# Performance work log

Hardware: AMD Instinct MI355X
Metric: run time of the kernel (lower is better)

## Reference

```python
import jax, jax.numpy as jnp
import numpy as np

L, B, D, H, DM = 4, 32768, 64, 256, 32
NS = 8            # fixed RK4 steps standing in for adaptive Dormand-Prince (atol=1e-5)
EPS = 1e-3        # keras BatchNormalization epsilon


def setup_inputs() -> dict:
    key = jax.random.key(0)
    ks = jax.random.split(key, 16)
    g = lambda k, shape, s=0.05: jax.random.normal(k, shape, jnp.float32) * s
    perm = jnp.concatenate([jnp.arange(DM, D), jnp.arange(DM)]).astype(jnp.int32)
    return {
        'x': jax.random.normal(ks[0], (B, D), jnp.float32),
        'perms': jnp.tile(perm[None, :], (L, 1)),
        'nvp_W0': g(ks[1], (L, DM, H)), 'nvp_b0': jnp.zeros((L, H), jnp.float32),
        'nvp_W1': g(ks[2], (L, H, H)), 'nvp_b1': jnp.zeros((L, H), jnp.float32),
        'nvp_W2': g(ks[3], (L, H, 2 * (D - DM))), 'nvp_b2': jnp.zeros((L, 2 * (D - DM)), jnp.float32),
        'ode_W0': g(ks[4], (L, D + 1, H)), 'ode_b0': jnp.zeros((L, H), jnp.float32),
        'ode_W1': g(ks[5], (L, H, H)), 'ode_b1': jnp.zeros((L, H), jnp.float32),
        'ode_W2': g(ks[6], (L, H, D)), 'ode_b2': jnp.zeros((L, D), jnp.float32),
        'bn1_mean': g(ks[7], (L, D), 0.1), 'bn1_var': jax.random.uniform(ks[8], (L, D), jnp.float32, 0.5, 1.5),
        'bn1_gamma': jax.random.uniform(ks[9], (L, D), jnp.float32, 0.8, 1.2), 'bn1_beta': g(ks[10], (L, D), 0.1),
        'bn2_mean': g(ks[11], (L, D), 0.1), 'bn2_var': jax.random.uniform(ks[12], (L, D), jnp.float32, 0.5, 1.5),
        'bn2_gamma': jax.random.uniform(ks[13], (L, D), jnp.float32, 0.8, 1.2), 'bn2_beta': g(ks[14], (L, D), 0.1),
    }


def _nvp(x, W0, b0, W1, b1, W2, b2):
    # RealNVP coupling: pass-through masked half, affine-transform the rest
    x0, x1 = x[:, :DM], x[:, DM:]
    h = jax.nn.relu(x0 @ W0 + b0)
    h = jax.nn.relu(h @ W1 + b1)
    shift, log_scale = jnp.split(h @ W2 + b2, 2, axis=-1)
    return jnp.concatenate([x0, x1 * jnp.exp(log_scale) + shift], axis=-1)


def _bn_fwd(x, mean, var, gamma, beta):
    # TFP BatchNormalization bijector forward == de-normalization
    return (x - beta) * jnp.sqrt(var + EPS) / gamma + mean


def _ffjord(x, W0, b0, W1, b1, W2, b2):
    # integrate dx/dt = MLP([t, x]) from t=0 to t=1 (fixed-step RK4)
    def f(t, y):
        ty = jnp.concatenate([jnp.full((y.shape[0], 1), t, y.dtype), y], axis=-1)
        h = jnp.tanh(ty @ W0 + b0)
        h = jnp.tanh(h @ W1 + b1)
        return h @ W2 + b2

    dt = 1.0 / NS

    def step(y, t):
        k1 = f(t, y)
        k2 = f(t + dt / 2, y + (dt / 2) * k1)
        k3 = f(t + dt / 2, y + (dt / 2) * k2)
        k4 = f(t + dt, y + dt * k3)
        return y + (dt / 6) * (k1 + 2 * k2 + 2 * k3 + k4), None

    ts = jnp.arange(NS, dtype=x.dtype) * dt
    y, _ = jax.lax.scan(step, x, ts)
    return y


def reference(x, perms, nvp_W0, nvp_b0, nvp_W1, nvp_b1, nvp_W2, nvp_b2,
              ode_W0, ode_b0, ode_W1, ode_b1, ode_W2, ode_b2,
              bn1_mean, bn1_var, bn1_gamma, bn1_beta,
              bn2_mean, bn2_var, bn2_gamma, bn2_beta):
    for i in range(L):  # per layer: Permute -> RealNVP -> BN -> FFJORD -> BN
        x = x[:, perms[i]]
        x = _nvp(x, nvp_W0[i], nvp_b0[i], nvp_W1[i], nvp_b1[i], nvp_W2[i], nvp_b2[i])
        x = _bn_fwd(x, bn1_mean[i], bn1_var[i], bn1_gamma[i], bn1_beta[i])
        x = _ffjord(x, ode_W0[i], ode_b0[i], ode_W1[i], ode_b1[i], ode_W2[i], ode_b2[i])
        x = _bn_fwd(x, bn2_mean[i], bn2_var[i], bn2_gamma[i], bn2_beta[i])
    return x
```

## Files before the change

### kernel.cpp

```cpp
#include <hip/hip_runtime.h>


#define LNUM   4
#define NSTEP  8
#define EPSV   1e-3f

typedef __attribute__((ext_vector_type(8))) short  short8;
typedef __attribute__((ext_vector_type(4))) float  floatx4;

#define MF(a, b, c) __builtin_amdgcn_mfma_f32_16x16x32_bf16((a), (b), (c), 0, 0, 0)

#define OW0_OFF 0
#define OW1_OFF 65536
#define OW2_OFF 327680
#define NW0_OFF 393216
#define NW1_OFF 425984
#define NW2_OFF 688128
#define WS_ELEMS 753664

#define W1B_OFF  0
#define H1_OFF   81920
#define H2_OFF   98304
#define YIN_OFF  114688
#define X1B_OFF  118784
#define SHF_OFF  120832
#define PARS_OFF 122880
#define LDS_SIZE 126208

__device__ __forceinline__ unsigned short f2bfu(float f) {
  return (unsigned short)((__float_as_uint(f) + 0x8000u) >> 16);
}

__device__ __forceinline__ unsigned short f2bfu_rne(float f) {
  unsigned int u = __float_as_uint(f);
  return (unsigned short)((u + 0x7FFFu + ((u >> 16) & 1u)) >> 16);
}

__device__ __forceinline__ unsigned long long pack4bf(float a, float b, float c, float d) {
  return (unsigned long long)f2bfu(a)
       | ((unsigned long long)f2bfu(b) << 16)
       | ((unsigned long long)f2bfu(c) << 32)
       | ((unsigned long long)f2bfu(d) << 48);
}

__device__ __forceinline__ float bfu2f(unsigned short u) {
  return __uint_as_float((unsigned int)u << 16);
}

__device__ __forceinline__ float tanh_fast(float x) {
  float e = __expf(2.0f * x);
  return 1.0f - 2.0f * __builtin_amdgcn_rcpf(e + 1.0f);
}

__global__ void prep_kernel(const float* __restrict__ odeW0, const float* __restrict__ odeW1,
                            const float* __restrict__ odeW2, const float* __restrict__ nvpW0,
                            const float* __restrict__ nvpW1, const float* __restrict__ nvpW2,
                            unsigned short* __restrict__ ws) {
  int idx = blockIdx.x * blockDim.x + threadIdx.x;
  if (idx >= WS_ELEMS) return;
  const float* W; int base, K, N, lstride, skip;
  int f = idx;
  if (f < OW1_OFF)      { W = odeW0; base = OW0_OFF; K = 64;  N = 256; lstride = 16640; skip = 1; f -= OW0_OFF; }
  else if (f < OW2_OFF) { W = odeW1; base = OW1_OFF; K = 256; N = 256; lstride = 65536; skip = 0; f -= OW1_OFF; }
  else if (f < NW0_OFF) { W = odeW2; base = OW2_OFF; K = 256; N = 64;  lstride = 16384; skip = 0; f -= OW2_OFF; }
  else if (f < NW1_OFF) { W = nvpW0; base = NW0_OFF; K = 32;  N = 256; lstride = 8192;  skip = 0; f -= NW0_OFF; }
  else if (f < NW2_OFF) { W = nvpW1; base = NW1_OFF; K = 256; N = 256; lstride = 65536; skip = 0; f -= NW1_OFF; }
  else                  { W = nvpW2; base = NW2_OFF; K = 256; N = 64;  lstride = 16384; skip = 0; f -= NW2_OFF; }
  int per   = K * N;
  int layer = f / per;
  int e     = f - layer * per;
  int j  = e & 7;
  int l  = (e >> 3) & 63;
  int t  = e >> 9;
  int KS = K >> 5; if (KS < 1) KS = 1;
  int ks = t % KS;
  int nt = t / KS;
  int n = nt * 16 + (l & 15);
  int k = ks * 32 + ((l >> 4) << 3) + j;
  ws[base + layer * per + e] = f2bfu_rne(W[layer * lstride + (k + skip) * N + n]);
}

__device__ __forceinline__ void st_h(char* dst, int m, int n0, float a, float b, float c, float d) {
  int off = (m * 512 + n0 * 2) ^ ((m & 15) << 4);
  *reinterpret_cast<unsigned long long*>(dst + off) = pack4bf(a, b, c, d);
}

__global__ void
__launch_bounds__(512)
flow_kernel(const float* __restrict__ xin,
            const float* __restrict__ nvp_b0, const float* __restrict__ nvp_b1,
            const float* __restrict__ nvp_b2,
            const float* __restrict__ odeW0_full,
            const float* __restrict__ ode_b0, const float* __restrict__ ode_b1,
            const float* __restrict__ ode_b2,
            const float* __restrict__ bn1m, const float* __restrict__ bn1v,
            const float* __restrict__ bn1g, const float* __restrict__ bn1b,
            const float* __restrict__ bn2m, const float* __restrict__ bn2v,
            const float* __restrict__ bn2g, const float* __restrict__ bn2b,
            const unsigned short* __restrict__ ws,
            float* __restrict__ out) {
  __shared__ __align__(16) char smem[LDS_SIZE];
  short8* w1b = reinterpret_cast<short8*>(smem + W1B_OFF);
  char*  h1   = smem + H1_OFF;
  char*  h2   = smem + H2_OFF;
  char*  yinb = smem + YIN_OFF;
  char*  x1b  = smem + X1B_OFF;
  char*  shfb = smem + SHF_OFF;
  float* pars = reinterpret_cast<float*>(smem + PARS_OFF);

  const floatx4 zero4 = {0.f, 0.f, 0.f, 0.f};

  const int tid  = threadIdx.x;
  const int lane = tid & 63;
  const int w    = tid >> 6;
  const int l15  = lane & 15;
  const int g    = lane >> 4;
  const int wn   = w & 3;
  const int wm   = w >> 2;
  const int nb   = w * 32;
  const int mrow = wm * 16 + l15;
  const int row0 = blockIdx.x * 32;
  const int d0   = wn * 16 + g * 4;
  const float dtv = 1.0f / NSTEP;

  float y[4];
  {
    floatx4 v = *reinterpret_cast<const floatx4*>(xin + (row0 + mrow) * 64 + d0);
    y[0] = v[0]; y[1] = v[1]; y[2] = v[2]; y[3] = v[3];
  }

  short8 aw0[2][2];
  short8 aw1h[2][3];
  short8 aw2[8];

  for (int l = 0; l < LNUM; ++l) {
    __syncthreads();
    {
      const short8* src = reinterpret_cast<const short8*>(ws + NW1_OFF + l * 65536);
      #pragma unroll 2
      for (int i = tid; i < 5120; i += 512) {
        int ks3 = i >> 10;
        int rem = i & 1023;
        w1b[i] = src[((rem >> 6) << 9) + ((3 + ks3) << 6) + (rem & 63)];
      }
    }
    if (wn >= 2) {
      int off = (mrow * 128 + (d0 - 32) * 2) ^ ((mrow & 7) << 4);
      *reinterpret_cast<unsigned long long*>(yinb + off) = pack4bf(y[0], y[1], y[2], y[3]);
    } else {
      int off = (mrow * 64 + d0 * 2) ^ ((mrow & 3) << 4);
      *reinterpret_cast<unsigned long long*>(x1b + off) = pack4bf(y[0], y[1], y[2], y[3]);
    }
    for (int i = tid; i < 576; i += 512) {
      float v;
      if (i < 256)      v = nvp_b0[l * 256 + i];
      else if (i < 512) v = nvp_b1[l * 256 + i - 256];
      else              v = nvp_b2[l * 64 + i - 512];
      pars[i] = v;
    }
    {
      const short8* p0 = reinterpret_cast<const short8*>(ws + NW0_OFF + l * 8192);
      const short8* p1 = reinterpret_cast<const short8*>(ws + NW1_OFF + l * 65536);
      const short8* p2 = reinterpret_cast<const short8*>(ws + NW2_OFF + l * 16384);
      aw0[0][0] = p0[(w * 2 + 0) * 64 + lane];
      aw0[1][0] = p0[(w * 2 + 1) * 64 + lane];
      #pragma unroll
      for (int nt = 0; nt < 2; ++nt)
        #pragma unroll
        for (int ks = 0; ks < 3; ++ks) aw1h[nt][ks] = p1[((w * 2 + nt) * 8 + ks) * 64 + lane];
      #pragma unroll
      for (int ks = 0; ks < 8; ++ks) aw2[ks] = p2[(wn * 8 + ks) * 64 + lane];
    }
    __syncthreads();

    {
      floatx4 acc[2][2];
      #pragma unroll
      for (int nt = 0; nt < 2; ++nt)
        #pragma unroll
        for (int mt = 0; mt < 2; ++mt) acc[nt][mt] = zero4;
      short8 B[2];
      #pragma unroll
      for (int mt = 0; mt < 2; ++mt) {
        int m = mt * 16 + l15;
        int off = (m * 128 + g * 16) ^ ((m & 7) << 4);
        B[mt] = *reinterpret_cast<const short8*>(yinb + off);
      }
      #pragma unroll
      for (int nt = 0; nt < 2; ++nt)
        #pragma unroll
        for (int mt = 0; mt < 2; ++mt) acc[nt][mt] = MF(aw0[nt][0], B[mt], acc[nt][mt]);
      #pragma unroll
      for (int nt = 0; nt < 2; ++nt) {
        int nbase = nb + nt * 16 + g * 4;
        floatx4 bb = *reinterpret_cast<const floatx4*>(pars + nbase);
        #pragma unroll
        for (int mt = 0; mt < 2; ++mt) {
          int m = mt * 16 + l15;
          st_h(h1, m, nbase,
               fmaxf(acc[nt][mt][0] + bb[0], 0.f), fmaxf(acc[nt][mt][1] + bb[1], 0.f),
               fmaxf(acc[nt][mt][2] + bb[2], 0.f), fmaxf(acc[nt][mt][3] + bb[3], 0.f));
        }
      }
    }
    __syncthreads();

    {
      floatx4 acc[2][2];
      #pragma unroll
      for (int nt = 0; nt < 2; ++nt)
        #pragma unroll
        for (int mt = 0; mt < 2; ++mt) acc[nt][mt] = zero4;
      #pragma unroll
      for (int ks = 0; ks < 8; ++ks) {
        short8 A[2], B[2];
        if (ks < 3) {
          A[0] = aw1h[0][ks]; A[1] = aw1h[1][ks];
        } else {
          A[0] = w1b[((ks - 3) << 10) + (w * 2 + 0) * 64 + lane];
          A[1] = w1b[((ks - 3) << 10) + (w * 2 + 1) * 64 + lane];
        }
        #pragma unroll
        for (int mt = 0; mt < 2; ++mt) {
          int m = mt * 16 + l15;
          int off = (m * 512 + (ks * 32 + g * 8) * 2) ^ ((m & 15) << 4);
          B[mt] = *reinterpret_cast<const short8*>(h1 + off);
        }
        #pragma unroll
        for (int nt = 0; nt < 2; ++nt)
          #pragma unroll
          for (int mt = 0; mt < 2; ++mt) acc[nt][mt] = MF(A[nt], B[mt], acc[nt][mt]);
      }
      #pragma unroll
      for (int nt = 0; nt < 2; ++nt) {
        int nbase = nb + nt * 16 + g * 4;
        floatx4 bb = *reinterpret_cast<const floatx4*>(pars + 256 + nbase);
        #pragma unroll
        for (int mt = 0; mt < 2; ++mt) {
          int m = mt * 16 + l15;
          st_h(h2, m, nbase,
               fmaxf(acc[nt][mt][0] + bb[0], 0.f), fmaxf(acc[nt][mt][1] + bb[1], 0.f),
               fmaxf(acc[nt][mt][2] + bb[2], 0.f), fmaxf(acc[nt][mt][3] + bb[3], 0.f));
        }
      }
    }
    __syncthreads();

    floatx4 a3 = zero4;
    #pragma unroll
    for (int ks = 0; ks < 8; ++ks) {
      int off = (mrow * 512 + (ks * 32 + g * 8) * 2) ^ ((mrow & 15) << 4);
      short8 B = *reinterpret_cast<const short8*>(h2 + off);
      a3 = MF(aw2[ks], B, a3);
    }
    {
      floatx4 b2v = *reinterpret_cast<const floatx4*>(pars + 512 + d0);
      #pragma unroll
      for (int p = 0; p < 4; ++p) a3[p] += b2v[p];
    }

    {
      const short8* src = reinterpret_cast<const short8*>(ws + OW1_OFF + l * 65536);
      #pragma unroll 2
      for (int i = tid; i < 5120; i += 512) {
        int ks3 = i >> 10;
        int rem = i & 1023;
        w1b[i] = src[((rem >> 6) << 9) + ((3 + ks3) << 6) + (rem & 63)];
      }
    }
    if (wn < 2) {
      int off = (mrow * 64 + d0 * 2) ^ ((mrow & 3) << 4);
      *reinterpret_cast<unsigned long long*>(shfb + off) = pack4bf(a3[0], a3[1], a3[2], a3[3]);
    }
    __syncthreads();

    if (wn < 2) {
      int off = (mrow * 128 + d0 * 2) ^ ((mrow & 7) << 4);
      unsigned long long u = *reinterpret_cast<const unsigned long long*>(yinb + off);
      y[0] = bfu2f((unsigned short)(u));
      y[1] = bfu2f((unsigned short)(u >> 16));
      y[2] = bfu2f((unsigned short)(u >> 32));
      y[3] = bfu2f((unsigned short)(u >> 48));
    } else {
      int offx = (mrow * 64 + (d0 - 32) * 2) ^ ((mrow & 3) << 4);
      unsigned long long ux = *reinterpret_cast<const unsigned long long*>(x1b + offx);
      unsigned long long us = *reinterpret_cast<const unsigned long long*>(shfb + offx);
      y[0] = bfu2f((unsigned short)(ux)) * __expf(a3[0]) + bfu2f((unsigned short)(us));
      y[1] = bfu2f((unsigned short)(ux >> 16)) * __expf(a3[1]) + bfu2f((unsigned short)(us >> 16));
      y[2] = bfu2f((unsigned short)(ux >> 32)) * __expf(a3[2]) + bfu2f((unsigned short)(us >> 32));
      y[3] = bfu2f((unsigned short)(ux >> 48)) * __expf(a3[3]) + bfu2f((unsigned short)(us >> 48));
    }
    {
      floatx4 mm = *reinterpret_cast<const floatx4*>(bn1m + l * 64 + d0);
      floatx4 vv = *reinterpret_cast<const floatx4*>(bn1v + l * 64 + d0);
      floatx4 gg = *reinterpret_cast<const floatx4*>(bn1g + l * 64 + d0);
      floatx4 be = *reinterpret_cast<const floatx4*>(bn1b + l * 64 + d0);
      #pragma unroll
      for (int p = 0; p < 4; ++p)
        y[p] = (y[p] - be[p]) * (sqrtf(vv[p] + EPSV) / gg[p]) + mm[p];
    }

    for (int i = tid; i < 832; i += 512) {
      float v;
      if (i < 256)      v = ode_b0[l * 256 + i];
      else if (i < 512) v = ode_b1[l * 256 + i - 256];
      else if (i < 576) v = ode_b2[l * 64 + i - 512];
      else              v = odeW0_full[l * 16640 + i - 576];
      pars[i] = v;
    }
    {
      const short8* p0 = reinterpret_cast<const short8*>(ws + OW0_OFF + l * 16384);
      const short8* p1 = reinterpret_cast<const short8*>(ws + OW1_OFF + l * 65536);
      const short8* p2 = reinterpret_cast<const short8*>(ws + OW2_OFF + l * 16384);
      #pragma unroll
      for (int nt = 0; nt < 2; ++nt)
        #pragma unroll
        for (int ks = 0; ks < 2; ++ks) aw0[nt][ks] = p0[((w * 2 + nt) * 2 + ks) * 64 + lane];
      #pragma unroll
      for (int nt = 0; nt < 2; ++nt)
        #pragma unroll
        for (int ks = 0; ks < 3; ++ks) aw1h[nt][ks] = p1[((w * 2 + nt) * 8 + ks) * 64 + lane];
      #pragma unroll
      for (int ks = 0; ks < 8; ++ks) aw2[ks] = p2[(wn * 8 + ks) * 64 + lane];
    }
    __syncthreads();

    float ka[4], kc[4];
    for (int s = 0; s < NSTEP; ++s) {
      float t0 = (float)s * dtv;
      for (int stg = 0; stg < 4; ++stg) {
        float cadd = (stg == 0) ? 0.0f : ((stg == 3) ? dtv : 0.5f * dtv);
        float tcur = t0 + cadd;
        {
          float v0, v1, v2, v3;
          if (stg == 0) { v0 = y[0]; v1 = y[1]; v2 = y[2]; v3 = y[3]; }
          else {
            v0 = fmaf(cadd, kc[0], y[0]); v1 = fmaf(cadd, kc[1], y[1]);
            v2 = fmaf(cadd, kc[2], y[2]); v3 = fmaf(cadd, kc[3], y[3]);
          }
          int off = (mrow * 128 + d0 * 2) ^ ((mrow & 7) << 4);
          *reinterpret_cast<unsigned long long*>(yinb + off) = pack4bf(v0, v1, v2, v3);
        }
        __syncthreads();

        {
          floatx4 acc[2][2];
          #pragma unroll
          for (int nt = 0; nt < 2; ++nt)
            #pragma unroll
            for (int mt = 0; mt < 2; ++mt) acc[nt][mt] = zero4;
          #pragma unroll
          for (int ks = 0; ks < 2; ++ks) {
            short8 B[2];
            #pragma unroll
            for (int mt = 0; mt < 2; ++mt) {
              int m = mt * 16 + l15;
              int off = (m * 128 + (ks * 32 + g * 8) * 2) ^ ((m & 7) << 4);
              B[mt] = *reinterpret_cast<const short8*>(yinb + off);
            }
            #pragma unroll
            for (int nt = 0; nt < 2; ++nt)
              #pragma unroll
              for (int mt = 0; mt < 2; ++mt) acc[nt][mt] = MF(aw0[nt][ks], B[mt], acc[nt][mt]);
          }
          #pragma unroll
          for (int nt = 0; nt < 2; ++nt) {
            int nbase = nb + nt * 16 + g * 4;
            floatx4 bb = *reinterpret_cast<const floatx4*>(pars + nbase);
            floatx4 w0 = *reinterpret_cast<const floatx4*>(pars + 576 + nbase);
            float c0 = bb[0] + tcur * w0[0], c1 = bb[1] + tcur * w0[1];
            float c2 = bb[2] + tcur * w0[2], c3 = bb[3] + tcur * w0[3];
            #pragma unroll
            for (int mt = 0; mt < 2; ++mt) {
              int m = mt * 16 + l15;
              st_h(h1, m, nbase,
                   tanh_fast(acc[nt][mt][0] + c0), tanh_fast(acc[nt][mt][1] + c1),
                   tanh_fast(acc[nt][mt][2] + c2), tanh_fast(acc[nt][mt][3] + c3));
            }
          }
        }
        __syncthreads();

        {
          floatx4 acc[2][2];
          #pragma unroll
          for (int nt = 0; nt < 2; ++nt)
            #pragma unroll
            for (int mt = 0; mt < 2; ++mt) acc[nt][mt] = zero4;
          #pragma unroll
          for (int ks = 0; ks < 8; ++ks) {
            short8 A[2], B[2];
            if (ks < 3) {
              A[0] = aw1h[0][ks]; A[1] = aw1h[1][ks];
            } else {
              A[0] = w1b[((ks - 3) << 10) + (w * 2 + 0) * 64 + lane];
              A[1] = w1b[((ks - 3) << 10) + (w * 2 + 1) * 64 + lane];
            }
            #pragma unroll
            for (int mt = 0; mt < 2; ++mt) {
              int m = mt * 16 + l15;
              int off = (m * 512 + (ks * 32 + g * 8) * 2) ^ ((m & 15) << 4);
              B[mt] = *reinterpret_cast<const short8*>(h1 + off);
            }
            #pragma unroll
            for (int nt = 0; nt < 2; ++nt)
              #pragma unroll
              for (int mt = 0; mt < 2; ++mt) acc[nt][mt] = MF(A[nt], B[mt], acc[nt][mt]);
          }
          #pragma unroll
          for (int nt = 0; nt < 2; ++nt) {
            int nbase = nb + nt * 16 + g * 4;
            floatx4 bb = *reinterpret_cast<const floatx4*>(pars + 256 + nbase);
            #pragma unroll
            for (int mt = 0; mt < 2; ++mt) {
              int m = mt * 16 + l15;
              st_h(h2, m, nbase,
                   tanh_fast(acc[nt][mt][0] + bb[0]), tanh_fast(acc[nt][mt][1] + bb[1]),
                   tanh_fast(acc[nt][mt][2] + bb[2]), tanh_fast(acc[nt][mt][3] + bb[3]));
            }
          }
        }
        __syncthreads();

        {
          floatx4 a2 = zero4;
          #pragma unroll
          for (int ks = 0; ks < 8; ++ks) {
            int off = (mrow * 512 + (ks * 32 + g * 8) * 2) ^ ((mrow & 15) << 4);
            short8 B = *reinterpret_cast<const short8*>(h2 + off);
            a2 = MF(aw2[ks], B, a2);
          }
          floatx4 b2v = *reinterpret_cast<const floatx4*>(pars + 512 + d0);
          #pragma unroll
          for (int p = 0; p < 4; ++p) kc[p] = a2[p] + b2v[p];
        }
        if (stg == 0) {
          #pragma unroll
          for (int i = 0; i < 4; ++i) ka[i] = kc[i];
        } else if (stg == 3) {
          #pragma unroll
          for (int i = 0; i < 4; ++i) ka[i] += kc[i];
        } else {
          #pragma unroll
          for (int i = 0; i < 4; ++i) ka[i] += 2.0f * kc[i];
        }
      }
      #pragma unroll
      for (int i = 0; i < 4; ++i) y[i] += (dtv / 6.0f) * ka[i];
    }

    {
      floatx4 mm = *reinterpret_cast<const floatx4*>(bn2m + l * 64 + d0);
      floatx4 vv = *reinterpret_cast<const floatx4*>(bn2v + l * 64 + d0);
      floatx4 gg = *reinterpret_cast<const floatx4*>(bn2g + l * 64 + d0);
      floatx4 be = *reinterpret_cast<const floatx4*>(bn2b + l * 64 + d0);
      #pragma unroll
      for (int p = 0; p < 4; ++p)
        y[p] = (y[p] - be[p]) * (sqrtf(vv[p] + EPSV) / gg[p]) + mm[p];
    }
  }

  {
    floatx4 v = {y[0], y[1], y[2], y[3]};
    *reinterpret_cast<floatx4*>(out + (row0 + mrow) * 64 + d0) = v;
  }
}

extern "C" void kernel_launch(void* const* d_in, const int* in_sizes, int n_in,
                              void* d_out, int out_size, void* d_ws, size_t ws_size,
                              hipStream_t stream) {
  const float* x      = (const float*)d_in[0];
  const float* nvpW0  = (const float*)d_in[2];
  const float* nvp_b0 = (const float*)d_in[3];
  const float* nvpW1  = (const float*)d_in[4];
  const float* nvp_b1 = (const float*)d_in[5];
  const float* nvpW2  = (const float*)d_in[6];
  const float* nvp_b2 = (const float*)d_in[7];
  const float* odeW0  = (const float*)d_in[8];
  const float* ode_b0 = (const float*)d_in[9];
  const float* odeW1  = (const float*)d_in[10];
  const float* ode_b1 = (const float*)d_in[11];
  const float* odeW2  = (const float*)d_in[12];
  const float* ode_b2 = (const float*)d_in[13];
  const float* bn1m   = (const float*)d_in[14];
  const float* bn1v   = (const float*)d_in[15];
  const float* bn1g   = (const float*)d_in[16];
  const float* bn1b   = (const float*)d_in[17];
  const float* bn2m   = (const float*)d_in[18];
  const float* bn2v   = (const float*)d_in[19];
  const float* bn2g   = (const float*)d_in[20];
  const float* bn2b   = (const float*)d_in[21];
  unsigned short* ws  = (unsigned short*)d_ws;
  float* out          = (float*)d_out;

  int pblocks = (WS_ELEMS + 255) / 256;
  prep_kernel<<<pblocks, 256, 0, stream>>>(odeW0, odeW1, odeW2, nvpW0, nvpW1, nvpW2, ws);
  flow_kernel<<<1024, 512, 0, stream>>>(x, nvp_b0, nvp_b1, nvp_b2, odeW0,
                                        ode_b0, ode_b1, ode_b2,
                                        bn1m, bn1v, bn1g, bn1b,
                                        bn2m, bn2v, bn2g, bn2b,
                                        ws, out);
}
```

Baseline: 1.326 ms.

## Process 64 rows per block to reuse register-resident weights over more rows

```diff
diff --git a/kernel.cpp b/kernel.cpp
--- a/kernel.cpp
+++ b/kernel.cpp
@@ -1,4 +1,5 @@
 #include <hip/hip_runtime.h>
+#include <hip/hip_bf16.h>
 
 
 #define LNUM   4
@@ -20,16 +21,10 @@
 
 #define W1B_OFF  0
 #define H1_OFF   81920
-#define H2_OFF   98304
-#define YIN_OFF  114688
-#define X1B_OFF  118784
-#define SHF_OFF  120832
-#define PARS_OFF 122880
-#define LDS_SIZE 126208
-
-__device__ __forceinline__ unsigned short f2bfu(float f) {
-  return (unsigned short)((__float_as_uint(f) + 0x8000u) >> 16);
-}
+#define H2_OFF   114688
+#define YIN_OFF  147456
+#define PARS_OFF 155648
+#define LDS_SIZE 158976
 
 __device__ __forceinline__ unsigned short f2bfu_rne(float f) {
   unsigned int u = __float_as_uint(f);
@@ -37,18 +32,20 @@
 }
 
 __device__ __forceinline__ unsigned long long pack4bf(float a, float b, float c, float d) {
-  return (unsigned long long)f2bfu(a)
-       | ((unsigned long long)f2bfu(b) << 16)
-       | ((unsigned long long)f2bfu(c) << 32)
-       | ((unsigned long long)f2bfu(d) << 48);
+  __hip_bfloat162 lo = __float22bfloat162_rn(make_float2(a, b));
+  __hip_bfloat162 hi = __float22bfloat162_rn(make_float2(c, d));
+  unsigned int ul, uh;
+  __builtin_memcpy(&ul, &lo, 4);
+  __builtin_memcpy(&uh, &hi, 4);
+  return (unsigned long long)ul | ((unsigned long long)uh << 32);
 }
 
 __device__ __forceinline__ float bfu2f(unsigned short u) {
   return __uint_as_float((unsigned int)u << 16);
 }
 
-__device__ __forceinline__ float tanh_fast(float x) {
-  float e = __expf(2.0f * x);
+__device__ __forceinline__ float tanh_fast2(float v) {
+  float e = __expf(v);
   return 1.0f - 2.0f * __builtin_amdgcn_rcpf(e + 1.0f);
 }
 
@@ -58,14 +55,14 @@
                             unsigned short* __restrict__ ws) {
   int idx = blockIdx.x * blockDim.x + threadIdx.x;
   if (idx >= WS_ELEMS) return;
-  const float* W; int base, K, N, lstride, skip;
+  const float* W; int base, K, N, lstride, skip; float scale;
   int f = idx;
-  if (f < OW1_OFF)      { W = odeW0; base = OW0_OFF; K = 64;  N = 256; lstride = 16640; skip = 1; f -= OW0_OFF; }
-  else if (f < OW2_OFF) { W = odeW1; base = OW1_OFF; K = 256; N = 256; lstride = 65536; skip = 0; f -= OW1_OFF; }
-  else if (f < NW0_OFF) { W = odeW2; base = OW2_OFF; K = 256; N = 64;  lstride = 16384; skip = 0; f -= OW2_OFF; }
-  else if (f < NW1_OFF) { W = nvpW0; base = NW0_OFF; K = 32;  N = 256; lstride = 8192;  skip = 0; f -= NW0_OFF; }
-  else if (f < NW2_OFF) { W = nvpW1; base = NW1_OFF; K = 256; N = 256; lstride = 65536; skip = 0; f -= NW1_OFF; }
-  else                  { W = nvpW2; base = NW2_OFF; K = 256; N = 64;  lstride = 16384; skip = 0; f -= NW2_OFF; }
+  if (f < OW1_OFF)      { W = odeW0; base = OW0_OFF; K = 64;  N = 256; lstride = 16640; skip = 1; scale = 2.f; f -= OW0_OFF; }
+  else if (f < OW2_OFF) { W = odeW1; base = OW1_OFF; K = 256; N = 256; lstride = 65536; skip = 0; scale = 2.f; f -= OW1_OFF; }
+  else if (f < NW0_OFF) { W = odeW2; base = OW2_OFF; K = 256; N = 64;  lstride = 16384; skip = 0; scale = 1.f; f -= OW2_OFF; }
+  else if (f < NW1_OFF) { W = nvpW0; base = NW0_OFF; K = 32;  N = 256; lstride = 8192;  skip = 0; scale = 1.f; f -= NW0_OFF; }
+  else if (f < NW2_OFF) { W = nvpW1; base = NW1_OFF; K = 256; N = 256; lstride = 65536; skip = 0; scale = 1.f; f -= NW1_OFF; }
+  else                  { W = nvpW2; base = NW2_OFF; K = 256; N = 64;  lstride = 16384; skip = 0; scale = 1.f; f -= NW2_OFF; }
   int per   = K * N;
   int layer = f / per;
   int e     = f - layer * per;
@@ -77,7 +74,7 @@
   int nt = t / KS;
   int n = nt * 16 + (l & 15);
   int k = ks * 32 + ((l >> 4) << 3) + j;
-  ws[base + layer * per + e] = f2bfu_rne(W[layer * lstride + (k + skip) * N + n]);
+  ws[base + layer * per + e] = f2bfu_rne(scale * W[layer * lstride + (k + skip) * N + n]);
 }
 
 __device__ __forceinline__ void st_h(char* dst, int m, int n0, float a, float b, float c, float d) {
@@ -104,8 +101,7 @@
   char*  h1   = smem + H1_OFF;
   char*  h2   = smem + H2_OFF;
   char*  yinb = smem + YIN_OFF;
-  char*  x1b  = smem + X1B_OFF;
-  char*  shfb = smem + SHF_OFF;
+  char*  shfb = smem + H1_OFF;
   float* pars = reinterpret_cast<float*>(smem + PARS_OFF);
 
   const floatx4 zero4 = {0.f, 0.f, 0.f, 0.f};
@@ -118,15 +114,16 @@
   const int wn   = w & 3;
   const int wm   = w >> 2;
   const int nb   = w * 32;
-  const int mrow = wm * 16 + l15;
-  const int row0 = blockIdx.x * 32;
+  const int row0 = blockIdx.x * 64;
   const int d0   = wn * 16 + g * 4;
   const float dtv = 1.0f / NSTEP;
 
-  float y[4];
-  {
-    floatx4 v = *reinterpret_cast<const floatx4*>(xin + (row0 + mrow) * 64 + d0);
-    y[0] = v[0]; y[1] = v[1]; y[2] = v[2]; y[3] = v[3];
+  float y[8];
+  #pragma unroll
+  for (int mt = 0; mt < 2; ++mt) {
+    int m = wm * 32 + mt * 16 + l15;
+    floatx4 v = *reinterpret_cast<const floatx4*>(xin + (row0 + m) * 64 + d0);
+    y[mt * 4 + 0] = v[0]; y[mt * 4 + 1] = v[1]; y[mt * 4 + 2] = v[2]; y[mt * 4 + 3] = v[3];
   }
 
   short8 aw0[2][2];
@@ -144,12 +141,18 @@
         w1b[i] = src[((rem >> 6) << 9) + ((3 + ks3) << 6) + (rem & 63)];
       }
     }
-    if (wn >= 2) {
-      int off = (mrow * 128 + (d0 - 32) * 2) ^ ((mrow & 7) << 4);
-      *reinterpret_cast<unsigned long long*>(yinb + off) = pack4bf(y[0], y[1], y[2], y[3]);
-    } else {
-      int off = (mrow * 64 + d0 * 2) ^ ((mrow & 3) << 4);
-      *reinterpret_cast<unsigned long long*>(x1b + off) = pack4bf(y[0], y[1], y[2], y[3]);
+    #pragma unroll
+    for (int mt = 0; mt < 2; ++mt) {
+      int m = wm * 32 + mt * 16 + l15;
+      if (wn >= 2) {
+        int off = (m * 128 + (d0 - 32) * 2) ^ ((m & 7) << 4);
+        *reinterpret_cast<unsigned long long*>(yinb + off) =
+            pack4bf(y[mt * 4 + 0], y[mt * 4 + 1], y[mt * 4 + 2], y[mt * 4 + 3]);
+      } else {
+        int off = (m * 128 + 64 + d0 * 2) ^ ((m & 7) << 4);
+        *reinterpret_cast<unsigned long long*>(yinb + off) =
+            pack4bf(y[mt * 4 + 0], y[mt * 4 + 1], y[mt * 4 + 2], y[mt * 4 + 3]);
+      }
     }
     for (int i = tid; i < 576; i += 512) {
       float v;
@@ -173,7 +176,8 @@
     }
     __syncthreads();
 
-    {
+    #pragma unroll
+    for (int mh = 0; mh < 2; ++mh) {
       floatx4 acc[2][2];
       #pragma unroll
       for (int nt = 0; nt < 2; ++nt)
@@ -182,7 +186,7 @@
       short8 B[2];
       #pragma unroll
       for (int mt = 0; mt < 2; ++mt) {
-        int m = mt * 16 + l15;
+        int m = mh * 32 + mt * 16 + l15;
         int off = (m * 128 + g * 16) ^ ((m & 7) << 4);
         B[mt] = *reinterpret_cast<const short8*>(yinb + off);
       }
@@ -196,7 +200,7 @@
         floatx4 bb = *reinterpret_cast<const floatx4*>(pars + nbase);
         #pragma unroll
         for (int mt = 0; mt < 2; ++mt) {
-          int m = mt * 16 + l15;
+          int m = mh * 32 + mt * 16 + l15;
           st_h(h1, m, nbase,
                fmaxf(acc[nt][mt][0] + bb[0], 0.f), fmaxf(acc[nt][mt][1] + bb[1], 0.f),
                fmaxf(acc[nt][mt][2] + bb[2], 0.f), fmaxf(acc[nt][mt][3] + bb[3], 0.f));
@@ -205,7 +209,8 @@
     }
     __syncthreads();
 
-    {
+    #pragma unroll
+    for (int mh = 0; mh < 2; ++mh) {
       floatx4 acc[2][2];
       #pragma unroll
       for (int nt = 0; nt < 2; ++nt)
@@ -222,7 +227,7 @@
         }
         #pragma unroll
         for (int mt = 0; mt < 2; ++mt) {
-          int m = mt * 16 + l15;
+          int m = mh * 32 + mt * 16 + l15;
           int off = (m * 512 + (ks * 32 + g * 8) * 2) ^ ((m & 15) << 4);
           B[mt] = *reinterpret_cast<const short8*>(h1 + off);
         }
@@ -237,7 +242,7 @@
         floatx4 bb = *reinterpret_cast<const floatx4*>(pars + 256 + nbase);
         #pragma unroll
         for (int mt = 0; mt < 2; ++mt) {
-          int m = mt * 16 + l15;
+          int m = mh * 32 + mt * 16 + l15;
           st_h(h2, m, nbase,
                fmaxf(acc[nt][mt][0] + bb[0], 0.f), fmaxf(acc[nt][mt][1] + bb[1], 0.f),
                fmaxf(acc[nt][mt][2] + bb[2], 0.f), fmaxf(acc[nt][mt][3] + bb[3], 0.f));
@@ -246,17 +251,24 @@
     }
     __syncthreads();
 
-    floatx4 a3 = zero4;
+    floatx4 a3[2];
+    a3[0] = zero4; a3[1] = zero4;
     #pragma unroll
     for (int ks = 0; ks < 8; ++ks) {
-      int off = (mrow * 512 + (ks * 32 + g * 8) * 2) ^ ((mrow & 15) << 4);
-      short8 B = *reinterpret_cast<const short8*>(h2 + off);
-      a3 = MF(aw2[ks], B, a3);
+      #pragma unroll
+      for (int mt = 0; mt < 2; ++mt) {
+        int m = wm * 32 + mt * 16 + l15;
+        int off = (m * 512 + (ks * 32 + g * 8) * 2) ^ ((m & 15) << 4);
+        short8 B = *reinterpret_cast<const short8*>(h2 + off);
+        a3[mt] = MF(aw2[ks], B, a3[mt]);
+      }
     }
     {
       floatx4 b2v = *reinterpret_cast<const floatx4*>(pars + 512 + d0);
       #pragma unroll
-      for (int p = 0; p < 4; ++p) a3[p] += b2v[p];
+      for (int mt = 0; mt < 2; ++mt)
+        #pragma unroll
+        for (int p = 0; p < 4; ++p) a3[mt][p] += b2v[p];
     }
 
     {
@@ -269,43 +281,58 @@
       }
     }
     if (wn < 2) {
-      int off = (mrow * 64 + d0 * 2) ^ ((mrow & 3) << 4);
-      *reinterpret_cast<unsigned long long*>(shfb + off) = pack4bf(a3[0], a3[1], a3[2], a3[3]);
+      #pragma unroll
+      for (int mt = 0; mt < 2; ++mt) {
+        int m = wm * 32 + mt * 16 + l15;
+        int off = (m * 64 + d0 * 2) ^ ((m & 3) << 4);
+        *reinterpret_cast<unsigned long long*>(shfb + off) =
+            pack4bf(a3[mt][0], a3[mt][1], a3[mt][2], a3[mt][3]);
+      }
     }
     __syncthreads();
 
-    if (wn < 2) {
-      int off = (mrow * 128 + d0 * 2) ^ ((mrow & 7) << 4);
-      unsigned long long u = *reinterpret_cast<const unsigned long long*>(yinb + off);
-      y[0] = bfu2f((unsigned short)(u));
-      y[1] = bfu2f((unsigned short)(u >> 16));
-      y[2] = bfu2f((unsigned short)(u >> 32));
-      y[3] = bfu2f((unsigned short)(u >> 48));
-    } else {
-      int offx = (mrow * 64 + (d0 - 32) * 2) ^ ((mrow & 3) << 4);
-      unsigned long long ux = *reinterpret_cast<const unsigned long long*>(x1b + offx);
-      unsigned long long us = *reinterpret_cast<const unsigned long long*>(shfb + offx);
-      y[0] = bfu2f((unsigned short)(ux)) * __expf(a3[0]) + bfu2f((unsigned short)(us));
-      y[1] = bfu2f((unsigned short)(ux >> 16)) * __expf(a3[1]) + bfu2f((unsigned short)(us >> 16));
-      y[2] = bfu2f((unsigned short)(ux >> 32)) * __expf(a3[2]) + bfu2f((unsigned short)(us >> 32));
-      y[3] = bfu2f((unsigned short)(ux >> 48)) * __expf(a3[3]) + bfu2f((unsigned short)(us >> 48));
+    #pragma unroll
+    for (int mt = 0; mt < 2; ++mt) {
+      int m = wm * 32 + mt * 16 + l15;
+      if (wn < 2) {
+        int off = (m * 128 + d0 * 2) ^ ((m & 7) << 4);
+        unsigned long long u = *reinterpret_cast<const unsigned long long*>(yinb + off);
+        y[mt * 4 + 0] = bfu2f((unsigned short)(u));
+        y[mt * 4 + 1] = bfu2f((unsigned short)(u >> 16));
+        y[mt * 4 + 2] = bfu2f((unsigned short)(u >> 32));
+        y[mt * 4 + 3] = bfu2f((unsigned short)(u >> 48));
+      } else {
+        int offx = (m * 128 + 64 + (d0 - 32) * 2) ^ ((m & 7) << 4);
+        unsigned long long ux = *reinterpret_cast<const unsigned long long*>(yinb + offx);
+        int offs = (m * 64 + (d0 - 32) * 2) ^ ((m & 3) << 4);
+        unsigned long long us = *reinterpret_cast<const unsigned long long*>(shfb + offs);
+        y[mt * 4 + 0] = bfu2f((unsigned short)(ux)) * __expf(a3[mt][0]) + bfu2f((unsigned short)(us));
+        y[mt * 4 + 1] = bfu2f((unsigned short)(ux >> 16)) * __expf(a3[mt][1]) + bfu2f((unsigned short)(us >> 16));
+        y[mt * 4 + 2] = bfu2f((unsigned short)(ux >> 32)) * __expf(a3[mt][2]) + bfu2f((unsigned short)(us >> 32));
+        y[mt * 4 + 3] = bfu2f((unsigned short)(ux >> 48)) * __expf(a3[mt][3]) + bfu2f((unsigned short)(us >> 48));
+      }
     }
     {
       floatx4 mm = *reinterpret_cast<const floatx4*>(bn1m + l * 64 + d0);
       floatx4 vv = *reinterpret_cast<const floatx4*>(bn1v + l * 64 + d0);
       floatx4 gg = *reinterpret_cast<const floatx4*>(bn1g + l * 64 + d0);
       floatx4 be = *reinterpret_cast<const floatx4*>(bn1b + l * 64 + d0);
-      #pragma unroll
-      for (int p = 0; p < 4; ++p)
-        y[p] = (y[p] - be[p]) * (sqrtf(vv[p] + EPSV) / gg[p]) + mm[p];
+      float sc[4];
+      #pragma unroll
+      for (int p = 0; p < 4; ++p) sc[p] = sqrtf(vv[p] + EPSV) / gg[p];
+      #pragma unroll
+      for (int mt = 0; mt < 2; ++mt)
+        #pragma unroll
+        for (int p = 0; p < 4; ++p)
+          y[mt * 4 + p] = (y[mt * 4 + p] - be[p]) * sc[p] + mm[p];
     }
 
     for (int i = tid; i < 832; i += 512) {
       float v;
-      if (i < 256)      v = ode_b0[l * 256 + i];
-      else if (i < 512) v = ode_b1[l * 256 + i - 256];
+      if (i < 256)      v = 2.f * ode_b0[l * 256 + i];
+      else if (i < 512) v = 2.f * ode_b1[l * 256 + i - 256];
       else if (i < 576) v = ode_b2[l * 64 + i - 512];
-      else              v = odeW0_full[l * 16640 + i - 576];
+      else              v = 2.f * odeW0_full[l * 16640 + i - 576];
       pars[i] = v;
     }
     {
@@ -325,25 +352,31 @@
     }
     __syncthreads();
 
-    float ka[4], kc[4];
+    float ka[8], kc[8];
     for (int s = 0; s < NSTEP; ++s) {
       float t0 = (float)s * dtv;
       for (int stg = 0; stg < 4; ++stg) {
         float cadd = (stg == 0) ? 0.0f : ((stg == 3) ? dtv : 0.5f * dtv);
         float tcur = t0 + cadd;
-        {
+        #pragma unroll
+        for (int mt = 0; mt < 2; ++mt) {
+          int m = wm * 32 + mt * 16 + l15;
           float v0, v1, v2, v3;
-          if (stg == 0) { v0 = y[0]; v1 = y[1]; v2 = y[2]; v3 = y[3]; }
-          else {
-            v0 = fmaf(cadd, kc[0], y[0]); v1 = fmaf(cadd, kc[1], y[1]);
-            v2 = fmaf(cadd, kc[2], y[2]); v3 = fmaf(cadd, kc[3], y[3]);
+          if (stg == 0) {
+            v0 = y[mt * 4 + 0]; v1 = y[mt * 4 + 1]; v2 = y[mt * 4 + 2]; v3 = y[mt * 4 + 3];
+          } else {
+            v0 = fmaf(cadd, kc[mt * 4 + 0], y[mt * 4 + 0]);
+            v1 = fmaf(cadd, kc[mt * 4 + 1], y[mt * 4 + 1]);
+            v2 = fmaf(cadd, kc[mt * 4 + 2], y[mt * 4 + 2]);
+            v3 = fmaf(cadd, kc[mt * 4 + 3], y[mt * 4 + 3]);
           }
-          int off = (mrow * 128 + d0 * 2) ^ ((mrow & 7) << 4);
+          int off = (m * 128 + d0 * 2) ^ ((m & 7) << 4);
           *reinterpret_cast<unsigned long long*>(yinb + off) = pack4bf(v0, v1, v2, v3);
         }
         __syncthreads();
 
-        {
+        #pragma unroll
+        for (int mh = 0; mh < 2; ++mh) {
           floatx4 acc[2][2];
           #pragma unroll
           for (int nt = 0; nt < 2; ++nt)
@@ -354,7 +387,7 @@
             short8 B[2];
             #pragma unroll
             for (int mt = 0; mt < 2; ++mt) {
-              int m = mt * 16 + l15;
+              int m = mh * 32 + mt * 16 + l15;
               int off = (m * 128 + (ks * 32 + g * 8) * 2) ^ ((m & 7) << 4);
               B[mt] = *reinterpret_cast<const short8*>(yinb + off);
             }
@@ -372,16 +405,17 @@
             float c2 = bb[2] + tcur * w0[2], c3 = bb[3] + tcur * w0[3];
             #pragma unroll
             for (int mt = 0; mt < 2; ++mt) {
-              int m = mt * 16 + l15;
+              int m = mh * 32 + mt * 16 + l15;
               st_h(h1, m, nbase,
-                   tanh_fast(acc[nt][mt][0] + c0), tanh_fast(acc[nt][mt][1] + c1),
-                   tanh_fast(acc[nt][mt][2] + c2), tanh_fast(acc[nt][mt][3] + c3));
+                   tanh_fast2(acc[nt][mt][0] + c0), tanh_fast2(acc[nt][mt][1] + c1),
+                   tanh_fast2(acc[nt][mt][2] + c2), tanh_fast2(acc[nt][mt][3] + c3));
             }
           }
         }
         __syncthreads();
 
-        {
+        #pragma unroll
+        for (int mh = 0; mh < 2; ++mh) {
           floatx4 acc[2][2];
           #pragma unroll
           for (int nt = 0; nt < 2; ++nt)
@@ -398,7 +432,7 @@
             }
             #pragma unroll
             for (int mt = 0; mt < 2; ++mt) {
-              int m = mt * 16 + l15;
+              int m = mh * 32 + mt * 16 + l15;
               int off = (m * 512 + (ks * 32 + g * 8) * 2) ^ ((m & 15) << 4);
               B[mt] = *reinterpret_cast<const short8*>(h1 + off);
             }
@@ -413,40 +447,48 @@
             floatx4 bb = *reinterpret_cast<const floatx4*>(pars + 256 + nbase);
             #pragma unroll
             for (int mt = 0; mt < 2; ++mt) {
-              int m = mt * 16 + l15;
+              int m = mh * 32 + mt * 16 + l15;
               st_h(h2, m, nbase,
-                   tanh_fast(acc[nt][mt][0] + bb[0]), tanh_fast(acc[nt][mt][1] + bb[1]),
-                   tanh_fast(acc[nt][mt][2] + bb[2]), tanh_fast(acc[nt][mt][3] + bb[3]));
+                   tanh_fast2(acc[nt][mt][0] + bb[0]), tanh_fast2(acc[nt][mt][1] + bb[1]),
+                   tanh_fast2(acc[nt][mt][2] + bb[2]), tanh_fast2(acc[nt][mt][3] + bb[3]));
             }
           }
         }
         __syncthreads();
 
         {
-          floatx4 a2 = zero4;
+          floatx4 a2[2];
+          a2[0] = zero4; a2[1] = zero4;
           #pragma unroll
           for (int ks = 0; ks < 8; ++ks) {
-            int off = (mrow * 512 + (ks * 32 + g * 8) * 2) ^ ((mrow & 15) << 4);
-            short8 B = *reinterpret_cast<const short8*>(h2 + off);
-            a2 = MF(aw2[ks], B, a2);
+            #pragma unroll
+            for (int mt = 0; mt < 2; ++mt) {
+              int m = wm * 32 + mt * 16 + l15;
+              int off = (m * 512 + (ks * 32 + g * 8) * 2) ^ ((m & 15) << 4);
+              short8 B = *reinterpret_cast<const short8*>(h2 + off);
+              a2[mt] = MF(aw2[ks], B, a2[mt]);
+            }
           }
           floatx4 b2v = *reinterpret_cast<const floatx4*>(pars + 512 + d0);
           #pragma unroll
-          for (int p = 0; p < 4; ++p) kc[p] = a2[p] + b2v[p];
+          for (int mt = 0; mt < 2; ++mt)
+            #pragma unroll
+            for (int p = 0; p < 4; ++p)
+              kc[mt * 4 + p] = a2[mt][p] + b2v[p];
         }
         if (stg == 0) {
           #pragma unroll
-          for (int i = 0; i < 4; ++i) ka[i] = kc[i];
+          for (int i = 0; i < 8; ++i) ka[i] = kc[i];
         } else if (stg == 3) {
           #pragma unroll
-          for (int i = 0; i < 4; ++i) ka[i] += kc[i];
+          for (int i = 0; i < 8; ++i) ka[i] += kc[i];
         } else {
           #pragma unroll
-          for (int i = 0; i < 4; ++i) ka[i] += 2.0f * kc[i];
-        }
-      }
-      #pragma unroll
-      for (int i = 0; i < 4; ++i) y[i] += (dtv / 6.0f) * ka[i];
+          for (int i = 0; i < 8; ++i) ka[i] += 2.0f * kc[i];
+        }
+      }
+      #pragma unroll
+      for (int i = 0; i < 8; ++i) y[i] += (dtv / 6.0f) * ka[i];
     }
 
     {
@@ -454,15 +496,22 @@
       floatx4 vv = *reinterpret_cast<const floatx4*>(bn2v + l * 64 + d0);
       floatx4 gg = *reinterpret_cast<const floatx4*>(bn2g + l * 64 + d0);
       floatx4 be = *reinterpret_cast<const floatx4*>(bn2b + l * 64 + d0);
-      #pragma unroll
-      for (int p = 0; p < 4; ++p)
-        y[p] = (y[p] - be[p]) * (sqrtf(vv[p] + EPSV) / gg[p]) + mm[p];
+      float sc[4];
+      #pragma unroll
+      for (int p = 0; p < 4; ++p) sc[p] = sqrtf(vv[p] + EPSV) / gg[p];
+      #pragma unroll
+      for (int mt = 0; mt < 2; ++mt)
+        #pragma unroll
+        for (int p = 0; p < 4; ++p)
+          y[mt * 4 + p] = (y[mt * 4 + p] - be[p]) * sc[p] + mm[p];
     }
   }
 
-  {
-    floatx4 v = {y[0], y[1], y[2], y[3]};
-    *reinterpret_cast<floatx4*>(out + (row0 + mrow) * 64 + d0) = v;
+  #pragma unroll
+  for (int mt = 0; mt < 2; ++mt) {
+    int m = wm * 32 + mt * 16 + l15;
+    floatx4 v = {y[mt * 4 + 0], y[mt * 4 + 1], y[mt * 4 + 2], y[mt * 4 + 3]};
+    *reinterpret_cast<floatx4*>(out + (row0 + m) * 64 + d0) = v;
   }
 }
 
@@ -495,9 +544,9 @@
 
   int pblocks = (WS_ELEMS + 255) / 256;
   prep_kernel<<<pblocks, 256, 0, stream>>>(odeW0, odeW1, odeW2, nvpW0, nvpW1, nvpW2, ws);
-  flow_kernel<<<1024, 512, 0, stream>>>(x, nvp_b0, nvp_b1, nvp_b2, odeW0,
-                                        ode_b0, ode_b1, ode_b2,
-                                        bn1m, bn1v, bn1g, bn1b,
-                                        bn2m, bn2v, bn2g, bn2b,
-                                        ws, out);
-}
+  flow_kernel<<<512, 512, 0, stream>>>(x, nvp_b0, nvp_b1, nvp_b2, odeW0,
+                                       ode_b0, ode_b1, ode_b2,
+                                       bn1m, bn1v, bn1g, bn1b,
+                                       bn2m, bn2v, bn2g, bn2b,
+                                       ws, out);
+}
```

After: 1.253 ms. 5.5% less time.
